# Kernel tuning notes

Measured on AMD Instinct MI355X. Metric: run time of the kernel, lower is better.

The kernel has to match this reference:

```python
import jax, jax.numpy as jnp
import numpy as np

H, D, E, S_E, P_E, N, B = 16, 48, 768, 384, 128, 768, 1

def _ln(x, g=None, b=None, eps=1e-5):
    mu = jnp.mean(x, axis=-1, keepdims=True)
    var = jnp.var(x, axis=-1, keepdims=True)
    y = (x - mu) * jax.lax.rsqrt(var + eps)
    if g is not None:
        y = y * g
    if b is not None:
        y = y + b
    return y

def setup_inputs() -> dict:
    key = jax.random.key(0)
    ks = jax.random.split(key, 16)
    sc_e = 1.0 / np.sqrt(E)
    sc_s = 1.0 / np.sqrt(S_E)
    sc_p = 1.0 / np.sqrt(P_E)
    return {
        "a": jax.random.normal(ks[0], (B, N, E), jnp.float32),
        "s": jax.random.normal(ks[1], (B, N, S_E), jnp.float32),
        "pair_rep": jax.random.normal(ks[2], (B, N, N, P_E), jnp.float32),
        "beta": jax.random.normal(ks[3], (B, N, N), jnp.float32),
        # AdaLN: sigmoid-gated scale and shift from s
        "w_ada_gamma": jax.random.normal(ks[4], (S_E, E), jnp.float32) * sc_s,
        "w_ada_beta": jax.random.normal(ks[5], (S_E, E), jnp.float32) * sc_s,
        # q/k/v projections, stored as [E, H, D]
        "wq": jax.random.normal(ks[6], (E, H, D), jnp.float32) * sc_e,
        "bq": jnp.zeros((H, D), jnp.float32),
        "wk": jax.random.normal(ks[7], (E, H, D), jnp.float32) * sc_e,
        "wv": jax.random.normal(ks[8], (E, H, D), jnp.float32) * sc_e,
        # pair bias: LayerNorm(P_E) + Linear(P_E -> H, no bias)
        "ln_pair_g": jnp.ones((P_E,), jnp.float32),
        "ln_pair_b": jnp.zeros((P_E,), jnp.float32),
        "w_pair": jax.random.normal(ks[9], (P_E, H), jnp.float32) * sc_p,
        # gate projection [E, H, D], no bias, sigmoid
        "w_gate": jax.random.normal(ks[10], (E, H, D), jnp.float32) * sc_e,
        # output projections
        "w_proj_a": jax.random.normal(ks[11], (E, E), jnp.float32) * sc_e,
        "w_out": jax.random.normal(ks[12], (S_E, E), jnp.float32) * sc_s,
        "b_out": jnp.full((E,), -2.0, jnp.float32),
    }

def reference(a, s, pair_rep, beta, w_ada_gamma, w_ada_beta, wq, bq, wk, wv,
              ln_pair_g, ln_pair_b, w_pair, w_gate, w_proj_a, w_out, b_out):
    # AdaLN: normalize a (no affine); gamma/beta conditioned on normalized s
    a_n = _ln(a)
    s_n = _ln(s)
    gamma = jax.nn.sigmoid(s_n @ w_ada_gamma)
    a_mod = gamma * a_n + s_n @ w_ada_beta            # [B,N,E]

    q = jnp.einsum('bne,ehd->bnhd', a_mod, wq) + bq   # [B,N,H,D]
    k = jnp.einsum('bne,ehd->bnhd', a_mod, wk)
    v = jnp.einsum('bne,ehd->bnhd', a_mod, wv)
    g = jax.nn.sigmoid(jnp.einsum('bne,ehd->bnhd', a_mod, w_gate))

    # per-head pair bias: LN(pair) @ w_pair + beta -> [B,H,N,N]
    b = jnp.einsum('bnmp,ph->bhnm', _ln(pair_rep, ln_pair_g, ln_pair_b), w_pair)
    b = b + beta[:, None, :, :]

    scale = 1.0 / np.sqrt(D)
    logits = jnp.einsum('bnhd,bmhd->bhnm', q, k) * scale + b
    weights = jax.nn.softmax(logits, axis=-1)         # [B,H,N,N]

    attn = jnp.einsum('bhnm,bmhd->bhnd', weights, v)
    attn = attn * jnp.moveaxis(g, -2, -3)             # gate per head
    attn = jnp.moveaxis(attn, -3, -2).reshape(a.shape[0], a.shape[1], H * D)
    out = attn @ w_proj_a                             # [B,N,E]
    out = jax.nn.sigmoid(s @ w_out + b_out) * out
    return out
```

## Files before the change

kernel.cpp:

```cpp
#include <hip/hip_runtime.h>
#include <hip/hip_bf16.h>

typedef __attribute__((ext_vector_type(8))) short short8;
typedef __attribute__((ext_vector_type(8))) unsigned short u16x8;
typedef __attribute__((ext_vector_type(4))) unsigned short u16x4;
typedef __attribute__((ext_vector_type(4))) float f32x4;

#define NTOK 768
#define ED   768
#define SD   384
#define PD   128
#define NH   16
#define DH   48

__device__ __forceinline__ unsigned short f2bf(float x) {
  unsigned u = __builtin_bit_cast(unsigned, x);
  u += 0x7FFFu + ((u >> 16) & 1u);
  return (unsigned short)(u >> 16);
}
__device__ __forceinline__ float bf2f(unsigned short b) {
  unsigned u = ((unsigned)b) << 16;
  return __builtin_bit_cast(float, u);
}
__device__ __forceinline__ float sigm(float x) { return 1.0f / (1.0f + __expf(-x)); }

__device__ __forceinline__ void gl2lds(const unsigned short* g, unsigned short* l) {
  __builtin_amdgcn_global_load_lds(
      (const __attribute__((address_space(1))) unsigned int*)g,
      (__attribute__((address_space(3))) unsigned int*)l, 16, 0, 0);
}

constexpr size_t SZ_SN   = (size_t)NTOK * SD * 2;
constexpr size_t OFF_SNH = 0;
constexpr size_t OFF_SNL = OFF_SNH + SZ_SN;
constexpr size_t OFF_SRH = OFF_SNL + SZ_SN;
constexpr size_t OFF_SRL = OFF_SRH + SZ_SN;
constexpr size_t OFF_GAM = OFF_SRL + SZ_SN;
constexpr size_t OFF_BET = OFF_GAM + 2359296;
constexpr size_t OFF_OG  = OFF_BET + 2359296;
constexpr size_t OFF_AMH = OFF_OG  + 2359296;
constexpr size_t OFF_AML = OFF_AMH + 1179648;
constexpr size_t OFF_QB  = OFF_AML + 1179648;
constexpr size_t OFF_KB  = OFF_QB  + 1179648;
constexpr size_t OFF_VT  = OFF_KB  + 1179648;
constexpr size_t OFF_GBUF= OFF_VT  + 1179648;
constexpr size_t OFF_AGH = OFF_GBUF+ 2359296;
constexpr size_t OFF_AGL = OFF_AGH + 1179648;
constexpr size_t OFF_WSMH= OFF_AGL + 1179648;
constexpr size_t OFF_WSML= OFF_WSMH+ 1769472;
constexpr size_t OFF_WQH = OFF_WSML+ 1769472;
constexpr size_t OFF_WQL = OFF_WQH + 4718592;
constexpr size_t OFF_WPH = OFF_WQL + 4718592;
constexpr size_t OFF_WPL = OFF_WPH + 1179648;
constexpr size_t OFF_GWH = OFF_WPL + 1179648;
constexpr size_t OFF_GWL = OFF_GWH + 4096;
constexpr size_t OFF_SGW = OFF_GWL + 4096;
constexpr size_t OFF_QKL = OFF_SGW + 4096;
constexpr size_t OFF_PB  = OFF_QKL + 37748736;
constexpr size_t WS_NEED = OFF_PB  + 18874368;

__global__ void k_setup(const float* __restrict__ ln_g, const float* __restrict__ ln_b,
                        const float* __restrict__ w_pair,
                        unsigned short* __restrict__ gw_hi, unsigned short* __restrict__ gw_lo,
                        float* __restrict__ sgw, float* __restrict__ bw) {
  const int tid = threadIdx.x;
  if (tid < 128) {
    float g = ln_g[tid];
    for (int hh = 0; hh < 16; ++hh) {
      float gwv = g * w_pair[tid * 16 + hh];
      unsigned short hb = f2bf(gwv);
      gw_hi[tid * 16 + hh] = hb;
      gw_lo[tid * 16 + hh] = f2bf(gwv - bf2f(hb));
    }
  }
  if (tid < 16) {
    float sv = 0.f, bb = 0.f;
    for (int p = 0; p < 128; ++p) {
      float w = w_pair[p * 16 + tid];
      sv += ln_g[p] * w;
      bb += ln_b[p] * w;
    }
    sgw[tid] = sv;
    bw[tid]  = bb;
  }
}

__global__ __launch_bounds__(256) void k_wcvt(
    const float* __restrict__ wag, const float* __restrict__ wab, const float* __restrict__ wo,
    const float* __restrict__ wq, const float* __restrict__ wk, const float* __restrict__ wv,
    const float* __restrict__ wg, const float* __restrict__ wp,
    unsigned short* __restrict__ wsmh, unsigned short* __restrict__ wsml,
    unsigned short* __restrict__ wqh, unsigned short* __restrict__ wql,
    unsigned short* __restrict__ wph, unsigned short* __restrict__ wpl) {
  const int id = blockIdx.z;
  const float* src; int Ksrc; unsigned short *dh, *dl; int n0; int Kd;
  switch (id) {
    case 0: src = wag; Ksrc = 384; dh = wsmh; dl = wsml; n0 = 0;    Kd = 384; break;
    case 1: src = wab; Ksrc = 384; dh = wsmh; dl = wsml; n0 = 768;  Kd = 384; break;
    case 2: src = wo;  Ksrc = 384; dh = wsmh; dl = wsml; n0 = 1536; Kd = 384; break;
    case 3: src = wq;  Ksrc = 768; dh = wqh;  dl = wql;  n0 = 0;    Kd = 768; break;
    case 4: src = wk;  Ksrc = 768; dh = wqh;  dl = wql;  n0 = 768;  Kd = 768; break;
    case 5: src = wv;  Ksrc = 768; dh = wqh;  dl = wql;  n0 = 1536; Kd = 768; break;
    case 6: src = wg;  Ksrc = 768; dh = wqh;  dl = wql;  n0 = 2304; Kd = 768; break;
    default: src = wp; Ksrc = 768; dh = wph;  dl = wpl;  n0 = 0;    Kd = 768; break;
  }
  const int kt = blockIdx.x, ntile = blockIdx.y;
  if (kt * 32 >= Ksrc) return;
  __shared__ float t[32][33];
  const int tid = threadIdx.x;
  const int r = tid >> 3, c4 = (tid & 7) * 4;
  float4 v = *(const float4*)(src + (size_t)(kt * 32 + r) * 768 + ntile * 32 + c4);
  t[r][c4 + 0] = v.x; t[r][c4 + 1] = v.y; t[r][c4 + 2] = v.z; t[r][c4 + 3] = v.w;
  __syncthreads();
  u16x4 hv, lv;
#pragma unroll
  for (int j = 0; j < 4; ++j) {
    float x = t[c4 + j][r];
    unsigned short hb = f2bf(x);
    hv[j] = hb;
    lv[j] = f2bf(x - bf2f(hb));
  }
  size_t drow = (size_t)(n0 + ntile * 32 + r) * Kd + kt * 32 + c4;
  *(u16x4*)(dh + drow) = hv;
  *(u16x4*)(dl + drow) = lv;
}

__global__ __launch_bounds__(64) void k_ln_s(const float* __restrict__ s,
                                             unsigned short* __restrict__ snh, unsigned short* __restrict__ snl,
                                             unsigned short* __restrict__ srh, unsigned short* __restrict__ srl) {
  const int n = blockIdx.x, lane = threadIdx.x;
  const float* row = s + (size_t)n * SD;
  float v[6], sum = 0.f, sq = 0.f;
#pragma unroll
  for (int i = 0; i < 6; ++i) { v[i] = row[lane + 64 * i]; sum += v[i]; sq += v[i] * v[i]; }
#pragma unroll
  for (int off = 1; off < 64; off <<= 1) { sum += __shfl_xor(sum, off); sq += __shfl_xor(sq, off); }
  float mu = sum * (1.f / SD);
  float var = sq * (1.f / SD) - mu * mu;
  float rs = rsqrtf(var + 1e-5f);
#pragma unroll
  for (int i = 0; i < 6; ++i) {
    size_t idx = (size_t)n * SD + lane + 64 * i;
    float x = v[i];
    unsigned short xh = f2bf(x);
    srh[idx] = xh; srl[idx] = f2bf(x - bf2f(xh));
    float y = (x - mu) * rs;
    unsigned short yh = f2bf(y);
    snh[idx] = yh; snl[idx] = f2bf(y - bf2f(yh));
  }
}

__device__ __forceinline__ void mfma_core(
    const unsigned short* __restrict__ Ah, const unsigned short* __restrict__ Al,
    const unsigned short* __restrict__ Bh, const unsigned short* __restrict__ Bl,
    int K, int mBase, int nBase, f32x4 acc[4][4]) {
  __shared__ unsigned short lds[2][4][8192];
  const int tid = threadIdx.x;
  const int w = tid >> 6, lane = tid & 63;
  const int l15 = lane & 15, kg = lane >> 4;
  const int wr = w >> 1, wc = w & 1;

  size_t offA[4], offB[4];
  int ldsw[4];
#pragma unroll
  for (int i = 0; i < 4; ++i) {
    int chunk = w * 256 + i * 64 + lane;
    int row = chunk >> 3;
    int slot = (chunk & 7) ^ (row & 7);
    offA[i] = (size_t)(mBase + row) * K + slot * 8;
    offB[i] = (size_t)(nBase + row) * K + slot * 8;
    ldsw[i] = w * 2048 + i * 512;
  }
  auto stage = [&](int b, int k0) {
#pragma unroll
    for (int i = 0; i < 4; ++i) {
      gl2lds(Ah + offA[i] + k0, &lds[b][0][ldsw[i]]);
      gl2lds(Al + offA[i] + k0, &lds[b][1][ldsw[i]]);
      gl2lds(Bh + offB[i] + k0, &lds[b][2][ldsw[i]]);
      gl2lds(Bl + offB[i] + k0, &lds[b][3][ldsw[i]]);
    }
  };

  stage(0, 0);
  int buf = 0;
  for (int k0 = 64; k0 <= K; k0 += 64) {
    __syncthreads();
    if (k0 < K) stage(buf ^ 1, k0);
#pragma unroll
    for (int kk = 0; kk < 2; ++kk) {
      short8 ah[4], al[4], bh4[4], bl4[4];
#pragma unroll
      for (int mi = 0; mi < 4; ++mi) {
        int row = wr * 64 + mi * 16 + l15;
        int kb = kk * 64 + kg * 16;
        int idx = row * 64 + ((kb ^ ((row & 7) << 4)) >> 1);
        ah[mi] = *(const short8*)&lds[buf][0][idx];
        al[mi] = *(const short8*)&lds[buf][1][idx];
      }
#pragma unroll
      for (int ni = 0; ni < 4; ++ni) {
        int row = wc * 64 + ni * 16 + l15;
        int kb = kk * 64 + kg * 16;
        int idx = row * 64 + ((kb ^ ((row & 7) << 4)) >> 1);
        bh4[ni] = *(const short8*)&lds[buf][2][idx];
        bl4[ni] = *(const short8*)&lds[buf][3][idx];
      }
#pragma unroll
      for (int mi = 0; mi < 4; ++mi)
#pragma unroll
        for (int ni = 0; ni < 4; ++ni) {
          acc[mi][ni] = __builtin_amdgcn_mfma_f32_16x16x32_bf16(ah[mi], bh4[ni], acc[mi][ni], 0, 0, 0);
          acc[mi][ni] = __builtin_amdgcn_mfma_f32_16x16x32_bf16(al[mi], bh4[ni], acc[mi][ni], 0, 0, 0);
          acc[mi][ni] = __builtin_amdgcn_mfma_f32_16x16x32_bf16(ah[mi], bl4[ni], acc[mi][ni], 0, 0, 0);
        }
    }
    buf ^= 1;
  }
}

__global__ __launch_bounds__(256) void k_gemm_small(
    const unsigned short* __restrict__ snh, const unsigned short* __restrict__ snl,
    const unsigned short* __restrict__ srh, const unsigned short* __restrict__ srl,
    const unsigned short* __restrict__ wsmh, const unsigned short* __restrict__ wsml,
    const float* __restrict__ bo,
    float* __restrict__ gaml, float* __restrict__ betl, float* __restrict__ og) {
  const int nt = blockIdx.x, mt = blockIdx.y;
  const unsigned short* Ah = (nt < 12) ? snh : srh;
  const unsigned short* Al = (nt < 12) ? snl : srl;
  f32x4 acc[4][4];
#pragma unroll
  for (int i = 0; i < 4; ++i)
#pragma unroll
    for (int j = 0; j < 4; ++j) acc[i][j] = (f32x4){0.f, 0.f, 0.f, 0.f};
  mfma_core(Ah, Al, wsmh, wsml, SD, mt * 128, nt * 128, acc);
  const int tid = threadIdx.x;
  const int w = tid >> 6, lane = tid & 63;
  const int l15 = lane & 15, kg = lane >> 4;
  const int wr = w >> 1, wc = w & 1;
#pragma unroll
  for (int mi = 0; mi < 4; ++mi)
#pragma unroll
    for (int ni = 0; ni < 4; ++ni) {
      int col = nt * 128 + wc * 64 + ni * 16 + l15;
#pragma unroll
      for (int r = 0; r < 4; ++r) {
        int row = mt * 128 + wr * 64 + mi * 16 + kg * 4 + r;
        float v = acc[mi][ni][r];
        if (col < 768) gaml[(size_t)row * ED + col] = v;
        else if (col < 1536) betl[(size_t)row * ED + col - 768] = v;
        else og[(size_t)row * ED + col - 1536] = sigm(v + bo[col - 1536]);
      }
    }
}

__global__ __launch_bounds__(256) void k_gemm_qkvg(
    const unsigned short* __restrict__ amh, const unsigned short* __restrict__ aml,
    const unsigned short* __restrict__ wqh, const unsigned short* __restrict__ wql,
    const float* __restrict__ bq,
    unsigned short* __restrict__ qb, unsigned short* __restrict__ kb,
    unsigned short* __restrict__ vT, float* __restrict__ gbuf) {
  const int nt = blockIdx.x, mt = blockIdx.y;
  f32x4 acc[4][4];
#pragma unroll
  for (int i = 0; i < 4; ++i)
#pragma unroll
    for (int j = 0; j < 4; ++j) acc[i][j] = (f32x4){0.f, 0.f, 0.f, 0.f};
  mfma_core(amh, aml, wqh, wql, ED, mt * 128, nt * 128, acc);
  const int tid = threadIdx.x;
  const int w = tid >> 6, lane = tid & 63;
  const int l15 = lane & 15, kg = lane >> 4;
  const int wr = w >> 1, wc = w & 1;
  const int sel = nt / 6;
#pragma unroll
  for (int mi = 0; mi < 4; ++mi)
#pragma unroll
    for (int ni = 0; ni < 4; ++ni) {
      int col = nt * 128 + wc * 64 + ni * 16 + l15;
      int c = col - sel * 768;
#pragma unroll
      for (int r = 0; r < 4; ++r) {
        int row = mt * 128 + wr * 64 + mi * 16 + kg * 4 + r;
        float v = acc[mi][ni][r];
        size_t idx = (size_t)row * ED + c;
        if (sel == 0) qb[idx] = f2bf(v + bq[c]);
        else if (sel == 1) kb[idx] = f2bf(v);
        else if (sel == 2) vT[(size_t)c * NTOK + row] = f2bf(v);
        else gbuf[idx] = sigm(v);
      }
    }
}

__global__ __launch_bounds__(256) void k_gemm_proj(
    const unsigned short* __restrict__ agh, const unsigned short* __restrict__ agl,
    const unsigned short* __restrict__ wph, const unsigned short* __restrict__ wpl,
    const float* __restrict__ og, float* __restrict__ out) {
  const int nt = blockIdx.x, mt = blockIdx.y;
  f32x4 acc[4][4];
#pragma unroll
  for (int i = 0; i < 4; ++i)
#pragma unroll
    for (int j = 0; j < 4; ++j) acc[i][j] = (f32x4){0.f, 0.f, 0.f, 0.f};
  mfma_core(agh, agl, wph, wpl, ED, mt * 128, nt * 128, acc);
  const int tid = threadIdx.x;
  const int w = tid >> 6, lane = tid & 63;
  const int l15 = lane & 15, kg = lane >> 4;
  const int wr = w >> 1, wc = w & 1;
#pragma unroll
  for (int mi = 0; mi < 4; ++mi)
#pragma unroll
    for (int ni = 0; ni < 4; ++ni) {
      int col = nt * 128 + wc * 64 + ni * 16 + l15;
#pragma unroll
      for (int r = 0; r < 4; ++r) {
        int row = mt * 128 + wr * 64 + mi * 16 + kg * 4 + r;
        size_t idx = (size_t)row * ED + col;
        out[idx] = acc[mi][ni][r] * og[idx];
      }
    }
}

__global__ __launch_bounds__(256) void k_amod(const float* __restrict__ a,
                                              const float* __restrict__ gamma_lin,
                                              const float* __restrict__ beta_lin,
                                              unsigned short* __restrict__ amh,
                                              unsigned short* __restrict__ aml) {
  __shared__ float red[8];
  const int n = blockIdx.x, tid = threadIdx.x;
  const int lane = tid & 63, wid = tid >> 6;
  const float* row = a + (size_t)n * ED;
  float v[3], sum = 0.f, sq = 0.f;
#pragma unroll
  for (int i = 0; i < 3; ++i) { v[i] = row[tid + 256 * i]; sum += v[i]; sq += v[i] * v[i]; }
#pragma unroll
  for (int off = 1; off < 64; off <<= 1) { sum += __shfl_xor(sum, off); sq += __shfl_xor(sq, off); }
  if (lane == 0) { red[wid] = sum; red[4 + wid] = sq; }
  __syncthreads();
  float S = red[0] + red[1] + red[2] + red[3];
  float Q = red[4] + red[5] + red[6] + red[7];
  float mu = S * (1.f / ED);
  float var = Q * (1.f / ED) - mu * mu;
  float rs = rsqrtf(var + 1e-5f);
#pragma unroll
  for (int i = 0; i < 3; ++i) {
    int e = tid + 256 * i;
    float an = (v[i] - mu) * rs;
    size_t idx = (size_t)n * ED + e;
    float val = sigm(gamma_lin[idx]) * an + beta_lin[idx];
    unsigned short h = f2bf(val);
    amh[idx] = h;
    aml[idx] = f2bf(val - bf2f(h));
  }
}

__global__ __launch_bounds__(256) void k_qkw(const unsigned short* __restrict__ qb,
                                             const unsigned short* __restrict__ kb,
                                             const float* __restrict__ beta,
                                             float* __restrict__ qkl) {
  const int mt = blockIdx.x, ntile = blockIdx.y, h = blockIdx.z;
  __shared__ unsigned short qs[64 * 72];
  __shared__ unsigned short ksm[64 * 72];
  const int tid = threadIdx.x;
  const int n0 = ntile * 64, m0 = mt * 64;
  for (int idx = tid; idx < 64 * 6; idx += 256) {
    int row = idx / 6, c = idx % 6;
    *(u16x8*)(qs + row * 72 + c * 8)  = *(const u16x8*)(qb + (size_t)(n0 + row) * ED + h * DH + c * 8);
    *(u16x8*)(ksm + row * 72 + c * 8) = *(const u16x8*)(kb + (size_t)(m0 + row) * ED + h * DH + c * 8);
  }
  u16x8 z = {0, 0, 0, 0, 0, 0, 0, 0};
  for (int idx = tid; idx < 64 * 2; idx += 256) {
    int row = idx / 2, c = idx % 2;
    *(u16x8*)(qs + row * 72 + 48 + c * 8) = z;
    *(u16x8*)(ksm + row * 72 + 48 + c * 8) = z;
  }
  __syncthreads();
  const int wv = tid >> 6, lane = tid & 63;
  const int l15 = lane & 15, kg = lane >> 4;
  f32x4 acc[4];
#pragma unroll
  for (int ct = 0; ct < 4; ++ct) acc[ct] = (f32x4){0.f, 0.f, 0.f, 0.f};
#pragma unroll
  for (int ks2 = 0; ks2 < 2; ++ks2) {
    short8 av = *(const short8*)(qs + (wv * 16 + l15) * 72 + ks2 * 32 + kg * 8);
#pragma unroll
    for (int ct = 0; ct < 4; ++ct) {
      short8 bv = *(const short8*)(ksm + (ct * 16 + l15) * 72 + ks2 * 32 + kg * 8);
      acc[ct] = __builtin_amdgcn_mfma_f32_16x16x32_bf16(av, bv, acc[ct], 0, 0, 0);
    }
  }
  const float scale = 0.14433756729740643f;
#pragma unroll
  for (int ct = 0; ct < 4; ++ct)
#pragma unroll
    for (int r = 0; r < 4; ++r) {
      int nn = n0 + wv * 16 + kg * 4 + r;
      int mm = m0 + ct * 16 + l15;
      qkl[((size_t)nn * NH + h) * NTOK + mm] =
          fmaf(acc[ct][r], scale, beta[(size_t)nn * NTOK + mm]);
    }
}

__global__ __launch_bounds__(256) void k_pairsm(const float* __restrict__ pair_rep,
                                                const float* __restrict__ qkl,
                                                const unsigned short* __restrict__ gw_hi,
                                                const unsigned short* __restrict__ gw_lo,
                                                const float* __restrict__ sgw, const float* __restrict__ bw,
                                                unsigned short* __restrict__ pb) {
  __shared__ float lg[16 * 776];
  const int n = blockIdx.x;
  const int tid = threadIdx.x;
  const int wv = tid >> 6, lane = tid & 63;
  const int l15 = lane & 15, kg = lane >> 4;

  {
    const float4* src = (const float4*)(qkl + (size_t)n * (NH * NTOK));
    for (int i = tid; i < 3072; i += 256) {
      float4 v = src[i];
      int h = i / 192;
      int m = (i - h * 192) * 4;
      *(float4*)&lg[h * 776 + m] = v;
    }
  }
  __syncthreads();

  short8 bh[4], bl[4];
#pragma unroll
  for (int ks = 0; ks < 4; ++ks)
#pragma unroll
    for (int j = 0; j < 8; ++j) {
      int p = ks * 32 + kg * 8 + j;
      bh[ks][j] = (short)gw_hi[p * 16 + l15];
      bl[ks][j] = (short)gw_lo[p * 16 + l15];
    }
  const float sg = sgw[l15], bwh = bw[l15];

  for (int ch = wv; ch < 48; ch += 4) {
    const int m_base = ch * 16;
    const int m = m_base + l15;
    const float* xp = pair_rep + ((size_t)n * NTOK + m) * PD;

    float xk[4][8];
    float sum = 0.f, sq = 0.f;
#pragma unroll
    for (int ks = 0; ks < 4; ++ks) {
      float4 u0 = *(const float4*)(xp + ks * 32 + kg * 8);
      float4 u1 = *(const float4*)(xp + ks * 32 + kg * 8 + 4);
      xk[ks][0] = u0.x; xk[ks][1] = u0.y; xk[ks][2] = u0.z; xk[ks][3] = u0.w;
      xk[ks][4] = u1.x; xk[ks][5] = u1.y; xk[ks][6] = u1.z; xk[ks][7] = u1.w;
#pragma unroll
      for (int j = 0; j < 8; ++j) { sum += xk[ks][j]; sq = fmaf(xk[ks][j], xk[ks][j], sq); }
    }
    sum += __shfl_xor(sum, 16); sum += __shfl_xor(sum, 32);
    sq  += __shfl_xor(sq, 16);  sq  += __shfl_xor(sq, 32);
    float mu = sum * (1.f / 128.f);
    float var = sq * (1.f / 128.f) - mu * mu;
    float rstd = rsqrtf(var + 1e-5f);

    f32x4 acc = {0.f, 0.f, 0.f, 0.f};
#pragma unroll
    for (int ks = 0; ks < 4; ++ks) {
      short8 ah, al;
#pragma unroll
      for (int j = 0; j < 8; ++j) {
        unsigned short hb = f2bf(xk[ks][j]);
        ah[j] = (short)hb;
        al[j] = (short)f2bf(xk[ks][j] - bf2f(hb));
      }
      acc = __builtin_amdgcn_mfma_f32_16x16x32_bf16(ah, bh[ks], acc, 0, 0, 0);
      acc = __builtin_amdgcn_mfma_f32_16x16x32_bf16(al, bh[ks], acc, 0, 0, 0);
      acc = __builtin_amdgcn_mfma_f32_16x16x32_bf16(ah, bl[ks], acc, 0, 0, 0);
    }
#pragma unroll
    for (int r = 0; r < 4; ++r) {
      int rowp = kg * 4 + r;
      float mu_r = __shfl(mu, rowp);
      float rs_r = __shfl(rstd, rowp);
      float val = rs_r * (acc[r] - mu_r * sg) + bwh;
      lg[l15 * 776 + m_base + rowp] += val;
    }
  }
  __syncthreads();

#pragma unroll
  for (int hh = 0; hh < 4; ++hh) {
    int h = wv * 4 + hh;
    float x[12];
#pragma unroll
    for (int i = 0; i < 12; ++i) x[i] = lg[h * 776 + lane + 64 * i];
    float mx = x[0];
#pragma unroll
    for (int t = 1; t < 12; ++t) mx = fmaxf(mx, x[t]);
#pragma unroll
    for (int off = 1; off < 64; off <<= 1) mx = fmaxf(mx, __shfl_xor(mx, off));
    float e[12], sm = 0.f;
#pragma unroll
    for (int t = 0; t < 12; ++t) { e[t] = __expf(x[t] - mx); sm += e[t]; }
#pragma unroll
    for (int off = 1; off < 64; off <<= 1) sm += __shfl_xor(sm, off);
    float inv = 1.0f / sm;
    unsigned short* dst = pb + ((size_t)h * NTOK + n) * NTOK;
#pragma unroll
    for (int i = 0; i < 12; ++i) dst[lane + 64 * i] = f2bf(e[i] * inv);
  }
}

__global__ __launch_bounds__(256) void k_pv(const unsigned short* __restrict__ wb,
                                            const unsigned short* __restrict__ vT,
                                            const float* __restrict__ gbuf,
                                            unsigned short* __restrict__ agh,
                                            unsigned short* __restrict__ agl) {
  const int ntile = blockIdx.x, h = blockIdx.y;
  const int n0 = ntile * 64;
  __shared__ unsigned short wsm[64 * 40];
  __shared__ unsigned short vtm[48 * 40];
  const int tid = threadIdx.x;
  const int wv = tid >> 6, lane = tid & 63, l15 = lane & 15, kg = lane >> 4;
  f32x4 acc[3];
#pragma unroll
  for (int dt = 0; dt < 3; ++dt) acc[dt] = (f32x4){0.f, 0.f, 0.f, 0.f};
  for (int k0 = 0; k0 < NTOK; k0 += 32) {
    __syncthreads();
    {
      int row = tid >> 2, c = tid & 3;
      *(u16x8*)(wsm + row * 40 + c * 8) =
          *(const u16x8*)(wb + ((size_t)h * NTOK + (n0 + row)) * NTOK + k0 + c * 8);
    }
    if (tid < 192) {
      int d = tid >> 2, c = tid & 3;
      *(u16x8*)(vtm + d * 40 + c * 8) =
          *(const u16x8*)(vT + (size_t)(h * DH + d) * NTOK + k0 + c * 8);
    }
    __syncthreads();
    short8 av = *(const short8*)(wsm + (wv * 16 + l15) * 40 + kg * 8);
#pragma unroll
    for (int dt = 0; dt < 3; ++dt) {
      short8 bv = *(const short8*)(vtm + (dt * 16 + l15) * 40 + kg * 8);
      acc[dt] = __builtin_amdgcn_mfma_f32_16x16x32_bf16(av, bv, acc[dt], 0, 0, 0);
    }
  }
#pragma unroll
  for (int dt = 0; dt < 3; ++dt)
#pragma unroll
    for (int r = 0; r < 4; ++r) {
      int nn = n0 + wv * 16 + kg * 4 + r;
      int col = h * DH + dt * 16 + l15;
      size_t idx = (size_t)nn * ED + col;
      float val = acc[dt][r] * gbuf[idx];
      unsigned short hb = f2bf(val);
      agh[idx] = hb;
      agl[idx] = f2bf(val - bf2f(hb));
    }
}

extern "C" void kernel_launch(void* const* d_in, const int* in_sizes, int n_in,
                              void* d_out, int out_size, void* d_ws, size_t ws_size,
                              hipStream_t stream) {
  const float* a    = (const float*)d_in[0];
  const float* s    = (const float*)d_in[1];
  const float* pair = (const float*)d_in[2];
  const float* beta = (const float*)d_in[3];
  const float* wag  = (const float*)d_in[4];
  const float* wab  = (const float*)d_in[5];
  const float* wq   = (const float*)d_in[6];
  const float* bq   = (const float*)d_in[7];
  const float* wk   = (const float*)d_in[8];
  const float* wvp  = (const float*)d_in[9];
  const float* lng  = (const float*)d_in[10];
  const float* lnb  = (const float*)d_in[11];
  const float* wpair= (const float*)d_in[12];
  const float* wg   = (const float*)d_in[13];
  const float* wproj= (const float*)d_in[14];
  const float* wo   = (const float*)d_in[15];
  const float* bo   = (const float*)d_in[16];
  float* out = (float*)d_out;

  if (ws_size < WS_NEED) return;

  char* ws = (char*)d_ws;
  unsigned short* snh  = (unsigned short*)(ws + OFF_SNH);
  unsigned short* snl  = (unsigned short*)(ws + OFF_SNL);
  unsigned short* srh  = (unsigned short*)(ws + OFF_SRH);
  unsigned short* srl  = (unsigned short*)(ws + OFF_SRL);
  float*          gaml = (float*)(ws + OFF_GAM);
  float*          betl = (float*)(ws + OFF_BET);
  float*          og   = (float*)(ws + OFF_OG);
  unsigned short* amh  = (unsigned short*)(ws + OFF_AMH);
  unsigned short* aml  = (unsigned short*)(ws + OFF_AML);
  unsigned short* qb   = (unsigned short*)(ws + OFF_QB);
  unsigned short* kb   = (unsigned short*)(ws + OFF_KB);
  unsigned short* vT   = (unsigned short*)(ws + OFF_VT);
  float*          gbuf = (float*)(ws + OFF_GBUF);
  unsigned short* agh  = (unsigned short*)(ws + OFF_AGH);
  unsigned short* agl  = (unsigned short*)(ws + OFF_AGL);
  unsigned short* wsmh = (unsigned short*)(ws + OFF_WSMH);
  unsigned short* wsml = (unsigned short*)(ws + OFF_WSML);
  unsigned short* wqh  = (unsigned short*)(ws + OFF_WQH);
  unsigned short* wql  = (unsigned short*)(ws + OFF_WQL);
  unsigned short* wph  = (unsigned short*)(ws + OFF_WPH);
  unsigned short* wpl  = (unsigned short*)(ws + OFF_WPL);
  unsigned short* gwh  = (unsigned short*)(ws + OFF_GWH);
  unsigned short* gwl  = (unsigned short*)(ws + OFF_GWL);
  float*          sgw  = (float*)(ws + OFF_SGW);
  float*          bw   = sgw + 16;
  float*          qkl  = (float*)(ws + OFF_QKL);
  unsigned short* pb   = (unsigned short*)(ws + OFF_PB);

  hipLaunchKernelGGL(k_setup, dim3(1), dim3(256), 0, stream, lng, lnb, wpair, gwh, gwl, sgw, bw);
  hipLaunchKernelGGL(k_wcvt, dim3(24, 24, 8), dim3(256), 0, stream,
                     wag, wab, wo, wq, wk, wvp, wg, wproj, wsmh, wsml, wqh, wql, wph, wpl);
  hipLaunchKernelGGL(k_ln_s, dim3(768), dim3(64), 0, stream, s, snh, snl, srh, srl);
  hipLaunchKernelGGL(k_gemm_small, dim3(18, 6), dim3(256), 0, stream,
                     snh, snl, srh, srl, wsmh, wsml, bo, gaml, betl, og);
  hipLaunchKernelGGL(k_amod, dim3(768), dim3(256), 0, stream, a, gaml, betl, amh, aml);
  hipLaunchKernelGGL(k_gemm_qkvg, dim3(24, 6), dim3(256), 0, stream,
                     amh, aml, wqh, wql, bq, qb, kb, vT, gbuf);
  hipLaunchKernelGGL(k_qkw, dim3(12, 12, 16), dim3(256), 0, stream, qb, kb, beta, qkl);
  hipLaunchKernelGGL(k_pairsm, dim3(768), dim3(256), 0, stream,
                     pair, qkl, gwh, gwl, sgw, bw, pb);
  hipLaunchKernelGGL(k_pv, dim3(12, 16), dim3(256), 0, stream, pb, vT, gbuf, agh, agl);
  hipLaunchKernelGGL(k_gemm_proj, dim3(6, 6), dim3(256), 0, stream,
                     agh, agl, wph, wpl, og, out);
}
```

Measured before the change: 212.6 us.

## Merge setup kernels into weight conversion and double-buffer pair loads in pairsm

Folds the pair-weight setup and the s LayerNorm kernels into the weight-conversion launch as an extra grid slice, which removes two kernel launches. In the pair-bias/softmax kernel, pair_rep chunks are now loaded through a register double buffer so the next chunk's global loads overlap the current chunk's LN and MFMA work. Packed v_cvt_pk_bf16_f32 replaces the manual bf16 split, and MFMA operands are swapped so results land row-contiguous in LDS. The kernel is also given an occupancy hint of 3 blocks, and the q/k LDS staging loop in k_qkw is simplified. The extra registers for double buffering and the launch-bounds hint may cause spills.

Measured after the change: 205.2 us. -3.5%, faster.

```diff
diff --git a/kernel.cpp b/kernel.cpp
--- a/kernel.cpp
+++ b/kernel.cpp
@@ -5,6 +5,7 @@
 typedef __attribute__((ext_vector_type(8))) unsigned short u16x8;
 typedef __attribute__((ext_vector_type(4))) unsigned short u16x4;
 typedef __attribute__((ext_vector_type(4))) float f32x4;
+typedef __attribute__((ext_vector_type(4))) unsigned u32x4;
 
 #define NTOK 768
 #define ED   768
@@ -23,6 +24,18 @@
   return __builtin_bit_cast(float, u);
 }
 __device__ __forceinline__ float sigm(float x) { return 1.0f / (1.0f + __expf(-x)); }
+
+__device__ __forceinline__ unsigned cvtpk(float a, float b) {
+  unsigned r;
+  asm("v_cvt_pk_bf16_f32 %0, %1, %2" : "=v"(r) : "v"(a), "v"(b));
+  return r;
+}
+__device__ __forceinline__ float lo2f(unsigned p) {
+  return __builtin_bit_cast(float, p << 16);
+}
+__device__ __forceinline__ float hi2f(unsigned p) {
+  return __builtin_bit_cast(float, p & 0xFFFF0000u);
+}
 
 __device__ __forceinline__ void gl2lds(const unsigned short* g, unsigned short* l) {
   __builtin_amdgcn_global_load_lds(
@@ -59,39 +72,68 @@
 constexpr size_t OFF_PB  = OFF_QKL + 37748736;
 constexpr size_t WS_NEED = OFF_PB  + 18874368;
 
-__global__ void k_setup(const float* __restrict__ ln_g, const float* __restrict__ ln_b,
-                        const float* __restrict__ w_pair,
-                        unsigned short* __restrict__ gw_hi, unsigned short* __restrict__ gw_lo,
-                        float* __restrict__ sgw, float* __restrict__ bw) {
-  const int tid = threadIdx.x;
-  if (tid < 128) {
-    float g = ln_g[tid];
-    for (int hh = 0; hh < 16; ++hh) {
-      float gwv = g * w_pair[tid * 16 + hh];
-      unsigned short hb = f2bf(gwv);
-      gw_hi[tid * 16 + hh] = hb;
-      gw_lo[tid * 16 + hh] = f2bf(gwv - bf2f(hb));
-    }
-  }
-  if (tid < 16) {
-    float sv = 0.f, bb = 0.f;
-    for (int p = 0; p < 128; ++p) {
-      float w = w_pair[p * 16 + tid];
-      sv += ln_g[p] * w;
-      bb += ln_b[p] * w;
-    }
-    sgw[tid] = sv;
-    bw[tid]  = bb;
-  }
-}
-
 __global__ __launch_bounds__(256) void k_wcvt(
     const float* __restrict__ wag, const float* __restrict__ wab, const float* __restrict__ wo,
     const float* __restrict__ wq, const float* __restrict__ wk, const float* __restrict__ wv,
     const float* __restrict__ wg, const float* __restrict__ wp,
+    const float* __restrict__ lng, const float* __restrict__ lnb,
+    const float* __restrict__ wpair, const float* __restrict__ s,
     unsigned short* __restrict__ wsmh, unsigned short* __restrict__ wsml,
     unsigned short* __restrict__ wqh, unsigned short* __restrict__ wql,
-    unsigned short* __restrict__ wph, unsigned short* __restrict__ wpl) {
+    unsigned short* __restrict__ wph, unsigned short* __restrict__ wpl,
+    unsigned short* __restrict__ gwh, unsigned short* __restrict__ gwl,
+    float* __restrict__ sgw, float* __restrict__ bw,
+    unsigned short* __restrict__ snh, unsigned short* __restrict__ snl,
+    unsigned short* __restrict__ srh, unsigned short* __restrict__ srl) {
+  const int tid = threadIdx.x;
+  if (blockIdx.z == 8) {
+    const int gid = blockIdx.y * 24 + blockIdx.x;
+    if (gid == 192) {
+      if (tid < 128) {
+        float g = lng[tid];
+        for (int hh = 0; hh < 16; ++hh) {
+          float gwv = g * wpair[tid * 16 + hh];
+          unsigned short hb = f2bf(gwv);
+          gwh[tid * 16 + hh] = hb;
+          gwl[tid * 16 + hh] = f2bf(gwv - bf2f(hb));
+        }
+      }
+      if (tid < 16) {
+        float sv = 0.f, bb = 0.f;
+        for (int p = 0; p < 128; ++p) {
+          float w = wpair[p * 16 + tid];
+          sv += lng[p] * w;
+          bb += lnb[p] * w;
+        }
+        sgw[tid] = sv;
+        bw[tid]  = bb;
+      }
+      return;
+    }
+    if (gid > 192) return;
+    const int n = gid * 4 + (tid >> 6);
+    const int lane = tid & 63;
+    const float* row = s + (size_t)n * SD;
+    float v[6], sum = 0.f, sq = 0.f;
+#pragma unroll
+    for (int i = 0; i < 6; ++i) { v[i] = row[lane + 64 * i]; sum += v[i]; sq += v[i] * v[i]; }
+#pragma unroll
+    for (int off = 1; off < 64; off <<= 1) { sum += __shfl_xor(sum, off); sq += __shfl_xor(sq, off); }
+    float mu = sum * (1.f / SD);
+    float var = sq * (1.f / SD) - mu * mu;
+    float rs = rsqrtf(var + 1e-5f);
+#pragma unroll
+    for (int i = 0; i < 6; ++i) {
+      size_t idx = (size_t)n * SD + lane + 64 * i;
+      float x = v[i];
+      unsigned short xh = f2bf(x);
+      srh[idx] = xh; srl[idx] = f2bf(x - bf2f(xh));
+      float y = (x - mu) * rs;
+      unsigned short yh = f2bf(y);
+      snh[idx] = yh; snl[idx] = f2bf(y - bf2f(yh));
+    }
+    return;
+  }
   const int id = blockIdx.z;
   const float* src; int Ksrc; unsigned short *dh, *dl; int n0; int Kd;
   switch (id) {
@@ -107,7 +149,6 @@
   const int kt = blockIdx.x, ntile = blockIdx.y;
   if (kt * 32 >= Ksrc) return;
   __shared__ float t[32][33];
-  const int tid = threadIdx.x;
   const int r = tid >> 3, c4 = (tid & 7) * 4;
   float4 v = *(const float4*)(src + (size_t)(kt * 32 + r) * 768 + ntile * 32 + c4);
   t[r][c4 + 0] = v.x; t[r][c4 + 1] = v.y; t[r][c4 + 2] = v.z; t[r][c4 + 3] = v.w;
@@ -123,31 +164,6 @@
   size_t drow = (size_t)(n0 + ntile * 32 + r) * Kd + kt * 32 + c4;
   *(u16x4*)(dh + drow) = hv;
   *(u16x4*)(dl + drow) = lv;
-}
-
-__global__ __launch_bounds__(64) void k_ln_s(const float* __restrict__ s,
-                                             unsigned short* __restrict__ snh, unsigned short* __restrict__ snl,
-                                             unsigned short* __restrict__ srh, unsigned short* __restrict__ srl) {
-  const int n = blockIdx.x, lane = threadIdx.x;
-  const float* row = s + (size_t)n * SD;
-  float v[6], sum = 0.f, sq = 0.f;
-#pragma unroll
-  for (int i = 0; i < 6; ++i) { v[i] = row[lane + 64 * i]; sum += v[i]; sq += v[i] * v[i]; }
-#pragma unroll
-  for (int off = 1; off < 64; off <<= 1) { sum += __shfl_xor(sum, off); sq += __shfl_xor(sq, off); }
-  float mu = sum * (1.f / SD);
-  float var = sq * (1.f / SD) - mu * mu;
-  float rs = rsqrtf(var + 1e-5f);
-#pragma unroll
-  for (int i = 0; i < 6; ++i) {
-    size_t idx = (size_t)n * SD + lane + 64 * i;
-    float x = v[i];
-    unsigned short xh = f2bf(x);
-    srh[idx] = xh; srl[idx] = f2bf(x - bf2f(xh));
-    float y = (x - mu) * rs;
-    unsigned short yh = f2bf(y);
-    snh[idx] = yh; snl[idx] = f2bf(y - bf2f(yh));
-  }
 }
 
 __device__ __forceinline__ void mfma_core(
@@ -361,16 +377,18 @@
   __shared__ unsigned short ksm[64 * 72];
   const int tid = threadIdx.x;
   const int n0 = ntile * 64, m0 = mt * 64;
-  for (int idx = tid; idx < 64 * 6; idx += 256) {
-    int row = idx / 6, c = idx % 6;
-    *(u16x8*)(qs + row * 72 + c * 8)  = *(const u16x8*)(qb + (size_t)(n0 + row) * ED + h * DH + c * 8);
-    *(u16x8*)(ksm + row * 72 + c * 8) = *(const u16x8*)(kb + (size_t)(m0 + row) * ED + h * DH + c * 8);
-  }
-  u16x8 z = {0, 0, 0, 0, 0, 0, 0, 0};
-  for (int idx = tid; idx < 64 * 2; idx += 256) {
-    int row = idx / 2, c = idx % 2;
-    *(u16x8*)(qs + row * 72 + 48 + c * 8) = z;
-    *(u16x8*)(ksm + row * 72 + 48 + c * 8) = z;
+  const u16x8 z = {0, 0, 0, 0, 0, 0, 0, 0};
+#pragma unroll
+  for (int it = 0; it < 2; ++it) {
+    int idx = tid + it * 256;
+    int row = idx >> 3, c = idx & 7;
+    u16x8 vq = z, vk = z;
+    if (c < 6) {
+      vq = *(const u16x8*)(qb + (size_t)(n0 + row) * ED + h * DH + c * 8);
+      vk = *(const u16x8*)(kb + (size_t)(m0 + row) * ED + h * DH + c * 8);
+    }
+    *(u16x8*)(qs + row * 72 + c * 8) = vq;
+    *(u16x8*)(ksm + row * 72 + c * 8) = vk;
   }
   __syncthreads();
   const int wv = tid >> 6, lane = tid & 63;
@@ -399,17 +417,29 @@
     }
 }
 
-__global__ __launch_bounds__(256) void k_pairsm(const float* __restrict__ pair_rep,
-                                                const float* __restrict__ qkl,
-                                                const unsigned short* __restrict__ gw_hi,
-                                                const unsigned short* __restrict__ gw_lo,
-                                                const float* __restrict__ sgw, const float* __restrict__ bw,
-                                                unsigned short* __restrict__ pb) {
+__global__ __launch_bounds__(256, 3) void k_pairsm(const float* __restrict__ pair_rep,
+                                                   const float* __restrict__ qkl,
+                                                   const unsigned short* __restrict__ gw_hi,
+                                                   const unsigned short* __restrict__ gw_lo,
+                                                   const float* __restrict__ sgw, const float* __restrict__ bw,
+                                                   unsigned short* __restrict__ pb) {
   __shared__ float lg[16 * 776];
   const int n = blockIdx.x;
   const int tid = threadIdx.x;
   const int wv = tid >> 6, lane = tid & 63;
   const int l15 = lane & 15, kg = lane >> 4;
+
+#define LOADCH(X, CH) do {                                                        \
+    const float* xp_ = pair_rep + ((size_t)n * NTOK + (CH) * 16 + l15) * PD + kg * 8; \
+    _Pragma("unroll")                                                             \
+    for (int q_ = 0; q_ < 4; ++q_) {                                              \
+      X[q_ * 2]     = *(const float4*)(xp_ + q_ * 32);                            \
+      X[q_ * 2 + 1] = *(const float4*)(xp_ + q_ * 32 + 4);                        \
+    }                                                                             \
+  } while (0)
+
+  float4 Xa[8], Xb[8];
+  LOADCH(Xa, wv);
 
   {
     const float4* src = (const float4*)(qkl + (size_t)n * (NH * NTOK));
@@ -420,7 +450,6 @@
       *(float4*)&lg[h * 776 + m] = v;
     }
   }
-  __syncthreads();
 
   short8 bh[4], bl[4];
 #pragma unroll
@@ -431,53 +460,64 @@
       bh[ks][j] = (short)gw_hi[p * 16 + l15];
       bl[ks][j] = (short)gw_lo[p * 16 + l15];
     }
-  const float sg = sgw[l15], bwh = bw[l15];
-
-  for (int ch = wv; ch < 48; ch += 4) {
-    const int m_base = ch * 16;
-    const int m = m_base + l15;
-    const float* xp = pair_rep + ((size_t)n * NTOK + m) * PD;
-
-    float xk[4][8];
-    float sum = 0.f, sq = 0.f;
-#pragma unroll
-    for (int ks = 0; ks < 4; ++ks) {
-      float4 u0 = *(const float4*)(xp + ks * 32 + kg * 8);
-      float4 u1 = *(const float4*)(xp + ks * 32 + kg * 8 + 4);
-      xk[ks][0] = u0.x; xk[ks][1] = u0.y; xk[ks][2] = u0.z; xk[ks][3] = u0.w;
-      xk[ks][4] = u1.x; xk[ks][5] = u1.y; xk[ks][6] = u1.z; xk[ks][7] = u1.w;
-#pragma unroll
-      for (int j = 0; j < 8; ++j) { sum += xk[ks][j]; sq = fmaf(xk[ks][j], xk[ks][j], sq); }
-    }
-    sum += __shfl_xor(sum, 16); sum += __shfl_xor(sum, 32);
-    sq  += __shfl_xor(sq, 16);  sq  += __shfl_xor(sq, 32);
-    float mu = sum * (1.f / 128.f);
-    float var = sq * (1.f / 128.f) - mu * mu;
-    float rstd = rsqrtf(var + 1e-5f);
-
-    f32x4 acc = {0.f, 0.f, 0.f, 0.f};
-#pragma unroll
-    for (int ks = 0; ks < 4; ++ks) {
-      short8 ah, al;
-#pragma unroll
-      for (int j = 0; j < 8; ++j) {
-        unsigned short hb = f2bf(xk[ks][j]);
-        ah[j] = (short)hb;
-        al[j] = (short)f2bf(xk[ks][j] - bf2f(hb));
-      }
-      acc = __builtin_amdgcn_mfma_f32_16x16x32_bf16(ah, bh[ks], acc, 0, 0, 0);
-      acc = __builtin_amdgcn_mfma_f32_16x16x32_bf16(al, bh[ks], acc, 0, 0, 0);
-      acc = __builtin_amdgcn_mfma_f32_16x16x32_bf16(ah, bl[ks], acc, 0, 0, 0);
-    }
-#pragma unroll
-    for (int r = 0; r < 4; ++r) {
-      int rowp = kg * 4 + r;
-      float mu_r = __shfl(mu, rowp);
-      float rs_r = __shfl(rstd, rowp);
-      float val = rs_r * (acc[r] - mu_r * sg) + bwh;
-      lg[l15 * 776 + m_base + rowp] += val;
-    }
-  }
+  float sgv[4], bwv[4];
+#pragma unroll
+  for (int r = 0; r < 4; ++r) { sgv[r] = sgw[kg * 4 + r]; bwv[r] = bw[kg * 4 + r]; }
+
+  __syncthreads();
+
+#define PROC(X, CH) do {                                                          \
+    float sum_ = 0.f, sq_ = 0.f;                                                  \
+    _Pragma("unroll")                                                             \
+    for (int q_ = 0; q_ < 8; ++q_) {                                              \
+      sum_ += X[q_].x + X[q_].y + X[q_].z + X[q_].w;                              \
+      sq_ = fmaf(X[q_].x, X[q_].x, sq_); sq_ = fmaf(X[q_].y, X[q_].y, sq_);       \
+      sq_ = fmaf(X[q_].z, X[q_].z, sq_); sq_ = fmaf(X[q_].w, X[q_].w, sq_);       \
+    }                                                                             \
+    sum_ += __shfl_xor(sum_, 16); sum_ += __shfl_xor(sum_, 32);                   \
+    sq_  += __shfl_xor(sq_, 16);  sq_  += __shfl_xor(sq_, 32);                    \
+    float mu_ = sum_ * (1.f / 128.f);                                             \
+    float rstd_ = rsqrtf(sq_ * (1.f / 128.f) - mu_ * mu_ + 1e-5f);                \
+    f32x4 acc_ = {0.f, 0.f, 0.f, 0.f};                                            \
+    _Pragma("unroll")                                                             \
+    for (int ks_ = 0; ks_ < 4; ++ks_) {                                           \
+      float4 u0_ = X[ks_ * 2], u1_ = X[ks_ * 2 + 1];                              \
+      unsigned p0_ = cvtpk(u0_.x, u0_.y), p1_ = cvtpk(u0_.z, u0_.w);              \
+      unsigned p2_ = cvtpk(u1_.x, u1_.y), p3_ = cvtpk(u1_.z, u1_.w);              \
+      float l0_ = u0_.x - lo2f(p0_), l1_ = u0_.y - hi2f(p0_);                     \
+      float l2_ = u0_.z - lo2f(p1_), l3_ = u0_.w - hi2f(p1_);                     \
+      float l4_ = u1_.x - lo2f(p2_), l5_ = u1_.y - hi2f(p2_);                     \
+      float l6_ = u1_.z - lo2f(p3_), l7_ = u1_.w - hi2f(p3_);                     \
+      unsigned q0_ = cvtpk(l0_, l1_), q1_ = cvtpk(l2_, l3_);                      \
+      unsigned q2_ = cvtpk(l4_, l5_), q3_ = cvtpk(l6_, l7_);                      \
+      u32x4 hp_ = {p0_, p1_, p2_, p3_}, lp_ = {q0_, q1_, q2_, q3_};               \
+      short8 ah_ = __builtin_bit_cast(short8, hp_);                               \
+      short8 al_ = __builtin_bit_cast(short8, lp_);                               \
+      acc_ = __builtin_amdgcn_mfma_f32_16x16x32_bf16(bh[ks_], ah_, acc_, 0, 0, 0);\
+      acc_ = __builtin_amdgcn_mfma_f32_16x16x32_bf16(bh[ks_], al_, acc_, 0, 0, 0);\
+      acc_ = __builtin_amdgcn_mfma_f32_16x16x32_bf16(bl[ks_], ah_, acc_, 0, 0, 0);\
+    }                                                                             \
+    _Pragma("unroll")                                                             \
+    for (int r_ = 0; r_ < 4; ++r_) {                                              \
+      float val_ = rstd_ * (acc_[r_] - mu_ * sgv[r_]) + bwv[r_];                  \
+      lg[(kg * 4 + r_) * 776 + (CH) * 16 + l15] += val_;                          \
+    }                                                                             \
+  } while (0)
+
+  LOADCH(Xb, wv + 4);   PROC(Xa, wv);
+  LOADCH(Xa, wv + 8);   PROC(Xb, wv + 4);
+  LOADCH(Xb, wv + 12);  PROC(Xa, wv + 8);
+  LOADCH(Xa, wv + 16);  PROC(Xb, wv + 12);
+  LOADCH(Xb, wv + 20);  PROC(Xa, wv + 16);
+  LOADCH(Xa, wv + 24);  PROC(Xb, wv + 20);
+  LOADCH(Xb, wv + 28);  PROC(Xa, wv + 24);
+  LOADCH(Xa, wv + 32);  PROC(Xb, wv + 28);
+  LOADCH(Xb, wv + 36);  PROC(Xa, wv + 32);
+  LOADCH(Xa, wv + 40);  PROC(Xb, wv + 36);
+  LOADCH(Xb, wv + 44);  PROC(Xa, wv + 40);
+                        PROC(Xb, wv + 44);
+#undef LOADCH
+#undef PROC
   __syncthreads();
 
 #pragma unroll
@@ -604,10 +644,10 @@
   float*          qkl  = (float*)(ws + OFF_QKL);
   unsigned short* pb   = (unsigned short*)(ws + OFF_PB);
 
-  hipLaunchKernelGGL(k_setup, dim3(1), dim3(256), 0, stream, lng, lnb, wpair, gwh, gwl, sgw, bw);
-  hipLaunchKernelGGL(k_wcvt, dim3(24, 24, 8), dim3(256), 0, stream,
-                     wag, wab, wo, wq, wk, wvp, wg, wproj, wsmh, wsml, wqh, wql, wph, wpl);
-  hipLaunchKernelGGL(k_ln_s, dim3(768), dim3(64), 0, stream, s, snh, snl, srh, srl);
+  hipLaunchKernelGGL(k_wcvt, dim3(24, 24, 9), dim3(256), 0, stream,
+                     wag, wab, wo, wq, wk, wvp, wg, wproj, lng, lnb, wpair, s,
+                     wsmh, wsml, wqh, wql, wph, wpl, gwh, gwl, sgw, bw,
+                     snh, snl, srh, srl);
   hipLaunchKernelGGL(k_gemm_small, dim3(18, 6), dim3(256), 0, stream,
                      snh, snl, srh, srl, wsmh, wsml, bo, gaml, betl, og);
   hipLaunchKernelGGL(k_amod, dim3(768), dim3(256), 0, stream, a, gaml, betl, amh, aml);
```
